# Performance work log

Measured on AMD Instinct MI355X. Metric: run time of the kernel, lower is better.

The kernel has to match this reference:

```python
import jax, jax.numpy as jnp
import numpy as np

N_NODES = 50000
N_EDGES = 800000  # includes N_NODES self-loops so every node has in-degree >= 1
D_IN = 64
D_OUT = 64


def setup_inputs() -> dict:
    key = jax.random.key(0)
    k_feat, k_src, k_dst, k_wt, k_wp = jax.random.split(key, 5)
    feat = jax.random.normal(k_feat, (N_NODES, D_IN), dtype=jnp.float32)
    n_rand = N_EDGES - N_NODES
    loops = jnp.arange(N_NODES, dtype=jnp.int64)
    src = jnp.concatenate([loops, jax.random.randint(k_src, (n_rand,), 0, N_NODES, dtype=jnp.int64)])
    dst = jnp.concatenate([loops, jax.random.randint(k_dst, (n_rand,), 0, N_NODES, dtype=jnp.int64)])
    scale = 1.0 / np.sqrt(D_IN)
    W_theta = jax.random.normal(k_wt, (D_IN, D_OUT), dtype=jnp.float32) * scale
    b_theta = jnp.zeros((D_OUT,), dtype=jnp.float32)
    W_phi = jax.random.normal(k_wp, (D_IN, D_OUT), dtype=jnp.float32) * scale
    b_phi = jnp.zeros((D_OUT,), dtype=jnp.float32)
    return {"feat": feat, "src": src, "dst": dst,
            "W_theta": W_theta, "b_theta": b_theta,
            "W_phi": W_phi, "b_phi": b_phi}


def reference(feat, src, dst, W_theta, b_theta, W_phi, b_phi):
    # Per-edge message: theta(x_dst - x_src)  [fn.v_sub_u then Dense theta]
    diff = feat[dst] - feat[src]                       # [E, D_in]
    theta_e = diff @ W_theta + b_theta                 # [E, D_out]
    # Per-destination-node term: phi(x_dst)  [Dense phi]
    phi = feat @ W_phi + b_phi                         # [N, D_out]
    e = theta_e + phi[dst]                             # [E, D_out]  (fn.e_add_v)
    # Scatter-max aggregation by destination node (fn.max)
    out = jax.ops.segment_max(e, dst, num_segments=feat.shape[0])  # [N, D_out]
    return out
```

## Files before the change

kernel.cpp:

```cpp
#include <hip/hip_runtime.h>
#include <hip/hip_bf16.h>

#define N_NODES 50000
#define N_EDGES 800000
#define D 64
#define NB 1563
#define BCAP 1024
#define CHUNK_E 4096
#define NSC 196
#define NSTRIP 3125
#define GEMM_BLKS 196
#define NWAVES 784
#define SPW 4
#define MSTR 65
#define WLSTR 72
#define NRES 7

typedef __attribute__((ext_vector_type(8))) short short8v;
typedef __attribute__((ext_vector_type(4))) float float4v;

__device__ __forceinline__ float b2f(unsigned short h) {
    return __uint_as_float(((unsigned)h) << 16);
}
__device__ __forceinline__ unsigned short f2b(float f) {
    __hip_bfloat16 t = __float2bfloat16(f);
    return *reinterpret_cast<unsigned short*>(&t);
}
__device__ __forceinline__ unsigned f2ord(float f) {
    unsigned u = __float_as_uint(f);
    return (u & 0x80000000u) ? ~u : (u | 0x80000000u);
}
__device__ __forceinline__ float ord2f(unsigned o) {
    return __uint_as_float((o & 0x80000000u) ? (o ^ 0x80000000u) : ~o);
}

__global__ __launch_bounds__(256)
void gemm_scatter(const void* __restrict__ featv,
                  const void* __restrict__ srcv, const void* __restrict__ dstv,
                  const void* __restrict__ Wtv, const void* __restrict__ btv,
                  const void* __restrict__ Wpv, const void* __restrict__ bpv,
                  unsigned* __restrict__ c_cur, unsigned* __restrict__ packed,
                  unsigned short* __restrict__ T16, void* __restrict__ outv) {
    __shared__ __align__(16) unsigned short wt_l[64 * WLSTR];
    __shared__ __align__(16) unsigned short wp_l[64 * WLSTR];
    __shared__ __align__(16) float bias_l[64];
    __shared__ unsigned h[NB];
    __shared__ unsigned sf[2];
    const int t = threadIdx.x;

    if (t < 64) {
        const unsigned short* p = (const unsigned short*)featv;
        float x = b2f(p[2 * t]);
        float a = fabsf(x);
        bool insane = !(a <= 64.f) || (x != 0.f && a < 9.3132e-10f);
        unsigned long long mm = __ballot(insane);
        if (t == 0) sf[0] = (__popcll(mm) >= 8) ? 1u : 0u;
    } else if (t < 128) {
        const int* s32 = (const int*)srcv;
        int v = s32[2 * (t - 64) + 1];
        unsigned long long mm = __ballot(v == 0);
        if (t == 64) sf[1] = (__popcll(mm) >= 32) ? 1u : 0u;
    }
    __syncthreads();
    const unsigned fp32mode = sf[0];
    const unsigned idx64 = sf[1];

    if (blockIdx.x < GEMM_BLKS) {
        if (fp32mode) {
#pragma unroll
            for (int i = 0; i < 16; ++i) {
                int e = i * 256 + t;
                int k = e >> 6, n = e & 63;
                wt_l[n * WLSTR + k] = f2b(((const float*)Wtv)[e]);
                wp_l[n * WLSTR + k] = f2b(((const float*)Wpv)[e]);
            }
        } else {
#pragma unroll
            for (int i = 0; i < 16; ++i) {
                int e = i * 256 + t;
                int k = e >> 6, n = e & 63;
                wt_l[n * WLSTR + k] = ((const unsigned short*)Wtv)[e];
                wp_l[n * WLSTR + k] = ((const unsigned short*)Wpv)[e];
            }
        }
        if (t < 64) {
            float bt_, bp_;
            if (fp32mode) {
                bt_ = ((const float*)btv)[t];
                bp_ = ((const float*)bpv)[t];
            } else {
                bt_ = b2f(((const unsigned short*)btv)[t]);
                bp_ = b2f(((const unsigned short*)bpv)[t]);
            }
            bias_l[t] = bt_ + bp_;
        }
        __syncthreads();

        const int lane = t & 63, wid = t >> 6;
        const int wave = blockIdx.x * 4 + wid;
        const int m = lane & 15, q = lane >> 4;
        short8v Wt0[4], Wt1[4], Wp0[4], Wp1[4];
        float4 bs4[4];
#pragma unroll
        for (int c = 0; c < 4; ++c) {
            const int col = 16 * c + m;
            Wt0[c] = *(const short8v*)&wt_l[col * WLSTR + q * 8];
            Wt1[c] = *(const short8v*)&wt_l[col * WLSTR + 32 + q * 8];
            Wp0[c] = *(const short8v*)&wp_l[col * WLSTR + q * 8];
            Wp1[c] = *(const short8v*)&wp_l[col * WLSTR + 32 + q * 8];
            bs4[c] = *(const float4*)&bias_l[16 * c + 4 * q];
        }

        float* Cf  = (float*)outv;
        unsigned short* Ch = (unsigned short*)outv;
        const float* Ff = (const float*)featv;
        const short* Fh = (const short*)featv;

        short8v A0, A1;
        float4 raw[8];
        int w = wave;
        {
            int wc = min(w, NSTRIP - 1);
            const short* fr = Fh + (wc * 16 + m) * D + q * 8;
            const float* frf = Ff + (wc * 16 + m) * D + q * 8;
            if (fp32mode) {
                raw[0] = *(const float4*)(frf);      raw[1] = *(const float4*)(frf + 4);
                raw[2] = *(const float4*)(frf + 32); raw[3] = *(const float4*)(frf + 36);
                A0 = (short8v){(short)f2b(raw[0].x), (short)f2b(raw[0].y), (short)f2b(raw[0].z), (short)f2b(raw[0].w),
                               (short)f2b(raw[1].x), (short)f2b(raw[1].y), (short)f2b(raw[1].z), (short)f2b(raw[1].w)};
                A1 = (short8v){(short)f2b(raw[2].x), (short)f2b(raw[2].y), (short)f2b(raw[2].z), (short)f2b(raw[2].w),
                               (short)f2b(raw[3].x), (short)f2b(raw[3].y), (short)f2b(raw[3].z), (short)f2b(raw[3].w)};
            } else {
                A0 = *(const short8v*)fr;
                A1 = *(const short8v*)(fr + 32);
            }
        }

#pragma unroll
        for (int s = 0; s < SPW; ++s) {
            const int wn = wave + (s + 1) * NWAVES;
            if (s + 1 < SPW) {
                int wc = min(wn, NSTRIP - 1);
                if (fp32mode) {
                    const float* frf = Ff + (wc * 16 + m) * D + q * 8;
                    raw[0] = *(const float4*)(frf);      raw[1] = *(const float4*)(frf + 4);
                    raw[2] = *(const float4*)(frf + 32); raw[3] = *(const float4*)(frf + 36);
                } else {
                    const short* fr = Fh + (wc * 16 + m) * D + q * 8;
                    A0 = *(const short8v*)fr;
                    A1 = *(const short8v*)(fr + 32);
                }
            }
            if (w < NSTRIP) {
                short8v Acur0, Acur1;
                if (s + 1 < SPW && !fp32mode) {
                    const short* fr = Fh + (w * 16 + m) * D + q * 8;
                    Acur0 = *(const short8v*)fr;
                    Acur1 = *(const short8v*)(fr + 32);
                } else {
                    Acur0 = A0; Acur1 = A1;
                }
                const int node = w * 16 + m;
                unsigned short* Trow = T16 + node * D;
#pragma unroll
                for (int c = 0; c < 4; ++c) {
                    float4v accT = (float4v){0.f, 0.f, 0.f, 0.f};
                    float4v accP = (float4v){bs4[c].x, bs4[c].y, bs4[c].z, bs4[c].w};
                    accT = __builtin_amdgcn_mfma_f32_16x16x32_bf16(Wt0[c], Acur0, accT, 0, 0, 0);
                    accT = __builtin_amdgcn_mfma_f32_16x16x32_bf16(Wt1[c], Acur1, accT, 0, 0, 0);
                    accP = __builtin_amdgcn_mfma_f32_16x16x32_bf16(Wp0[c], Acur0, accP, 0, 0, 0);
                    accP = __builtin_amdgcn_mfma_f32_16x16x32_bf16(Wp1[c], Acur1, accP, 0, 0, 0);
                    const int foff = 16 * c + 4 * q;
                    unsigned t0 = (unsigned)f2b(accT[0]) | ((unsigned)f2b(accT[1]) << 16);
                    unsigned t1 = (unsigned)f2b(accT[2]) | ((unsigned)f2b(accT[3]) << 16);
                    *(uint2*)(Trow + foff) = make_uint2(t0, t1);
                    if (fp32mode) {
                        *(float4*)(Cf + node * D + foff) =
                            make_float4(accT[0] + accP[0], accT[1] + accP[1],
                                        accT[2] + accP[2], accT[3] + accP[3]);
                    } else {
                        unsigned c0 = (unsigned)f2b(accT[0] + accP[0])
                                    | ((unsigned)f2b(accT[1] + accP[1]) << 16);
                        unsigned c1 = (unsigned)f2b(accT[2] + accP[2])
                                    | ((unsigned)f2b(accT[3] + accP[3]) << 16);
                        *(uint2*)(Ch + node * D + foff) = make_uint2(c0, c1);
                    }
                }
            }
            w = wn;
            if (fp32mode && s + 1 < SPW) {
                A0 = (short8v){(short)f2b(raw[0].x), (short)f2b(raw[0].y), (short)f2b(raw[0].z), (short)f2b(raw[0].w),
                               (short)f2b(raw[1].x), (short)f2b(raw[1].y), (short)f2b(raw[1].z), (short)f2b(raw[1].w)};
                A1 = (short8v){(short)f2b(raw[2].x), (short)f2b(raw[2].y), (short)f2b(raw[2].z), (short)f2b(raw[2].w),
                               (short)f2b(raw[3].x), (short)f2b(raw[3].y), (short)f2b(raw[3].z), (short)f2b(raw[3].w)};
            }
        }
    } else {
        for (int i = t; i < NB; i += 256) h[i] = 0;
        __syncthreads();
        const int base = (blockIdx.x - GEMM_BLKS) * CHUNK_E;
        unsigned pk[CHUNK_E / 256];
#pragma unroll
        for (int j = 0; j < CHUNK_E / 256; ++j) {
            int e = base + j * 256 + t;
            unsigned p = 0xFFFFFFFFu;
            if (e < N_EDGES) {
                int s, d;
                if (idx64) {
                    s = (int)((const long long*)srcv)[e];
                    d = (int)((const long long*)dstv)[e];
                } else {
                    s = ((const int*)srcv)[e];
                    d = ((const int*)dstv)[e];
                }
                s = min(max(s, 0), N_NODES - 1);
                d = min(max(d, 0), N_NODES - 1);
                if (s != d) {
                    p = ((unsigned)d << 16) | (unsigned)s;
                    atomicAdd(&h[d >> 5], 1u);
                }
            }
            pk[j] = p;
        }
        __syncthreads();
        {
            unsigned cc[NRES], off[NRES];
#pragma unroll
            for (int r = 0; r < NRES; ++r) {
                int i = r * 256 + t;
                cc[r] = (i < NB) ? h[i] : 0u;
            }
#pragma unroll
            for (int r = 0; r < NRES; ++r) {
                int i = r * 256 + t;
                off[r] = (i < NB && cc[r]) ? atomicAdd(&c_cur[i], cc[r]) : 0u;
            }
            __syncthreads();
#pragma unroll
            for (int r = 0; r < NRES; ++r) {
                int i = r * 256 + t;
                if (i < NB) h[i] = off[r];
            }
        }
        __syncthreads();
#pragma unroll
        for (int j = 0; j < CHUNK_E / 256; ++j) {
            unsigned p = pk[j];
            if (p != 0xFFFFFFFFu) {
                unsigned bkt = p >> 21;
                unsigned pos = atomicAdd(&h[bkt], 1u);
                if (pos < BCAP)
                    packed[bkt * BCAP + pos] = p;
            }
        }
    }
}

__global__ __launch_bounds__(256, 8)
void bucket_min(const unsigned* __restrict__ c_cur, const unsigned* __restrict__ packed,
                const unsigned short* __restrict__ T16, const void* __restrict__ featv,
                void* __restrict__ outv) {
    __shared__ unsigned mn[32 * MSTR];
    __shared__ unsigned sf0;
    const int t = threadIdx.x;
    const int b = blockIdx.x;
    const int node0 = b << 5;
    if (t < 64) {
        const unsigned short* p = (const unsigned short*)featv;
        float x = b2f(p[2 * t]);
        float a = fabsf(x);
        bool insane = !(a <= 64.f) || (x != 0.f && a < 9.3132e-10f);
        unsigned long long mm = __ballot(insane);
        if (t == 0) sf0 = (__popcll(mm) >= 8) ? 1u : 0u;
    }
    for (int sl = t; sl < 32 * 16; sl += 256) {
        const int row = sl >> 4;
        const int f4 = (sl & 15) << 2;
        unsigned* mp = &mn[row * MSTR + f4];
        if (node0 + row < N_NODES) {
            uint2 v = *(const uint2*)(T16 + (node0 + row) * D + f4);
            mp[0] = f2ord(b2f((unsigned short)v.x));
            mp[1] = f2ord(b2f((unsigned short)(v.x >> 16)));
            mp[2] = f2ord(b2f((unsigned short)v.y));
            mp[3] = f2ord(b2f((unsigned short)(v.y >> 16)));
        } else {
            mp[0] = mp[1] = mp[2] = mp[3] = 0xFFFFFFFFu;
        }
    }
    __syncthreads();
    const unsigned fp32mode = sf0;
    const int cnt = min((int)c_cur[b], BCAP);
    const unsigned* pb = packed + b * BCAP;
    const int lane = t & 63, wv = t >> 6;
    const int g = lane >> 3;
    const int fh = (lane & 7) << 3;
    int i = wv * 8 + g;
    for (; i + 32 < cnt; i += 64) {
        unsigned p0 = pb[i], p1 = pb[i + 32];
        uint4 v0 = *(const uint4*)(T16 + (int)(p0 & 0xFFFFu) * D + fh);
        uint4 v1 = *(const uint4*)(T16 + (int)(p1 & 0xFFFFu) * D + fh);
        unsigned* m0p = &mn[(int)((p0 >> 16) & 31u) * MSTR + fh];
        unsigned* m1p = &mn[(int)((p1 >> 16) & 31u) * MSTR + fh];
        atomicMin(m0p + 0, f2ord(b2f((unsigned short)v0.x)));
        atomicMin(m0p + 1, f2ord(b2f((unsigned short)(v0.x >> 16))));
        atomicMin(m0p + 2, f2ord(b2f((unsigned short)v0.y)));
        atomicMin(m0p + 3, f2ord(b2f((unsigned short)(v0.y >> 16))));
        atomicMin(m0p + 4, f2ord(b2f((unsigned short)v0.z)));
        atomicMin(m0p + 5, f2ord(b2f((unsigned short)(v0.z >> 16))));
        atomicMin(m0p + 6, f2ord(b2f((unsigned short)v0.w)));
        atomicMin(m0p + 7, f2ord(b2f((unsigned short)(v0.w >> 16))));
        atomicMin(m1p + 0, f2ord(b2f((unsigned short)v1.x)));
        atomicMin(m1p + 1, f2ord(b2f((unsigned short)(v1.x >> 16))));
        atomicMin(m1p + 2, f2ord(b2f((unsigned short)v1.y)));
        atomicMin(m1p + 3, f2ord(b2f((unsigned short)(v1.y >> 16))));
        atomicMin(m1p + 4, f2ord(b2f((unsigned short)v1.z)));
        atomicMin(m1p + 5, f2ord(b2f((unsigned short)(v1.z >> 16))));
        atomicMin(m1p + 6, f2ord(b2f((unsigned short)v1.w)));
        atomicMin(m1p + 7, f2ord(b2f((unsigned short)(v1.w >> 16))));
    }
    for (; i < cnt; i += 32) {
        unsigned p0 = pb[i];
        uint4 v0 = *(const uint4*)(T16 + (int)(p0 & 0xFFFFu) * D + fh);
        unsigned* m0p = &mn[(int)((p0 >> 16) & 31u) * MSTR + fh];
        atomicMin(m0p + 0, f2ord(b2f((unsigned short)v0.x)));
        atomicMin(m0p + 1, f2ord(b2f((unsigned short)(v0.x >> 16))));
        atomicMin(m0p + 2, f2ord(b2f((unsigned short)v0.y)));
        atomicMin(m0p + 3, f2ord(b2f((unsigned short)(v0.y >> 16))));
        atomicMin(m0p + 4, f2ord(b2f((unsigned short)v0.z)));
        atomicMin(m0p + 5, f2ord(b2f((unsigned short)(v0.z >> 16))));
        atomicMin(m0p + 6, f2ord(b2f((unsigned short)v0.w)));
        atomicMin(m0p + 7, f2ord(b2f((unsigned short)(v0.w >> 16))));
    }
    __syncthreads();
    for (int sl = t; sl < 32 * 16; sl += 256) {
        const int row = sl >> 4;
        const int node = node0 + row;
        if (node >= N_NODES) continue;
        const int f4 = (sl & 15) << 2;
        const unsigned* mp = &mn[row * MSTR + f4];
        float m0 = ord2f(mp[0]), m1 = ord2f(mp[1]);
        float m2 = ord2f(mp[2]), m3 = ord2f(mp[3]);
        if (fp32mode) {
            float4* C = (float4*)((float*)outv + node * D + f4);
            float4 c = *C;
            *C = make_float4(c.x - m0, c.y - m1, c.z - m2, c.w - m3);
        } else {
            unsigned short* C = (unsigned short*)outv + node * D + f4;
            uint2 c = *(uint2*)C;
            unsigned lo = (unsigned)f2b(b2f((unsigned short)c.x) - m0)
                        | ((unsigned)f2b(b2f((unsigned short)(c.x >> 16)) - m1) << 16);
            unsigned hi = (unsigned)f2b(b2f((unsigned short)c.y) - m2)
                        | ((unsigned)f2b(b2f((unsigned short)(c.y >> 16)) - m3) << 16);
            *(uint2*)C = make_uint2(lo, hi);
        }
    }
}

__global__ __launch_bounds__(256)
void zero_ccur(unsigned* __restrict__ c_cur) {
    int i = blockIdx.x * 256 + threadIdx.x;
    if (i < NB) c_cur[i] = 0;
}

extern "C" void kernel_launch(void* const* d_in, const int* in_sizes, int n_in,
                              void* d_out, int out_size, void* d_ws, size_t ws_size,
                              hipStream_t stream) {
    char* p = (char*)d_ws;
    unsigned*       c_cur  = (unsigned*)p;
    unsigned*       packed = (unsigned*)(p + 8192);
    unsigned short* T16    = (unsigned short*)(p + 8192 + 6402048);

    hipError_t e = hipMemsetAsync(c_cur, 0, NB * sizeof(unsigned), stream);
    if (e != hipSuccess)
        zero_ccur<<<(NB + 255) / 256, 256, 0, stream>>>(c_cur);

    gemm_scatter<<<GEMM_BLKS + NSC, 256, 0, stream>>>(d_in[0], d_in[1], d_in[2],
                                                      d_in[3], d_in[4], d_in[5], d_in[6],
                                                      c_cur, packed, T16, d_out);
    bucket_min<<<NB, 256, 0, stream>>>(c_cur, packed, T16, d_in[0], d_out);
}
```

Before: 113.4 us.

## Make every block do both GEMM strips and edge bucketing

Before, the fused kernel split its blocks into two kinds: GEMM blocks and edge-scatter blocks. Now every one of 512 blocks loads its slice of edge indices up front, computes up to two 16-node GEMM strips, then does local histogramming and the scatter into packed buckets. The aim is to balance work across all CUs and to hide the index-load latency behind the MFMA work. In exchange every block stages the weights into LDS, and register pressure rises from the held edge indices under launch_bounds(256,2).

```diff
diff --git a/kernel.cpp b/kernel.cpp
--- a/kernel.cpp
+++ b/kernel.cpp
@@ -6,15 +6,14 @@
 #define D 64
 #define NB 1563
 #define BCAP 1024
-#define CHUNK_E 4096
-#define NSC 196
 #define NSTRIP 3125
-#define GEMM_BLKS 196
-#define NWAVES 784
-#define SPW 4
 #define MSTR 65
 #define WLSTR 72
 #define NRES 7
+#define K1_BLKS 512
+#define WAVES_G 2048
+#define EPB1 1568
+#define EJ 7
 
 typedef __attribute__((ext_vector_type(8))) short short8v;
 typedef __attribute__((ext_vector_type(4))) float float4v;
@@ -34,7 +33,7 @@
     return __uint_as_float((o & 0x80000000u) ? (o ^ 0x80000000u) : ~o);
 }
 
-__global__ __launch_bounds__(256)
+__global__ __launch_bounds__(256, 2)
 void gemm_scatter(const void* __restrict__ featv,
                   const void* __restrict__ srcv, const void* __restrict__ dstv,
                   const void* __restrict__ Wtv, const void* __restrict__ btv,
@@ -61,43 +60,58 @@
         unsigned long long mm = __ballot(v == 0);
         if (t == 64) sf[1] = (__popcll(mm) >= 32) ? 1u : 0u;
     }
+    for (int i = t; i < NB; i += 256) h[i] = 0;
     __syncthreads();
     const unsigned fp32mode = sf[0];
     const unsigned idx64 = sf[1];
 
-    if (blockIdx.x < GEMM_BLKS) {
+    if (fp32mode) {
+#pragma unroll
+        for (int i = 0; i < 16; ++i) {
+            int e = i * 256 + t;
+            int k = e >> 6, n = e & 63;
+            wt_l[n * WLSTR + k] = f2b(((const float*)Wtv)[e]);
+            wp_l[n * WLSTR + k] = f2b(((const float*)Wpv)[e]);
+        }
+    } else {
+#pragma unroll
+        for (int i = 0; i < 16; ++i) {
+            int e = i * 256 + t;
+            int k = e >> 6, n = e & 63;
+            wt_l[n * WLSTR + k] = ((const unsigned short*)Wtv)[e];
+            wp_l[n * WLSTR + k] = ((const unsigned short*)Wpv)[e];
+        }
+    }
+    if (t < 64) {
+        float bt_, bp_;
         if (fp32mode) {
-#pragma unroll
-            for (int i = 0; i < 16; ++i) {
-                int e = i * 256 + t;
-                int k = e >> 6, n = e & 63;
-                wt_l[n * WLSTR + k] = f2b(((const float*)Wtv)[e]);
-                wp_l[n * WLSTR + k] = f2b(((const float*)Wpv)[e]);
-            }
+            bt_ = ((const float*)btv)[t];
+            bp_ = ((const float*)bpv)[t];
         } else {
-#pragma unroll
-            for (int i = 0; i < 16; ++i) {
-                int e = i * 256 + t;
-                int k = e >> 6, n = e & 63;
-                wt_l[n * WLSTR + k] = ((const unsigned short*)Wtv)[e];
-                wp_l[n * WLSTR + k] = ((const unsigned short*)Wpv)[e];
-            }
-        }
-        if (t < 64) {
-            float bt_, bp_;
-            if (fp32mode) {
-                bt_ = ((const float*)btv)[t];
-                bp_ = ((const float*)bpv)[t];
-            } else {
-                bt_ = b2f(((const unsigned short*)btv)[t]);
-                bp_ = b2f(((const unsigned short*)bpv)[t]);
-            }
-            bias_l[t] = bt_ + bp_;
-        }
-        __syncthreads();
-
+            bt_ = b2f(((const unsigned short*)btv)[t]);
+            bp_ = b2f(((const unsigned short*)bpv)[t]);
+        }
+        bias_l[t] = bt_ + bp_;
+    }
+
+    const int base = blockIdx.x * EPB1;
+    int es[EJ], ed[EJ];
+#pragma unroll
+    for (int j = 0; j < EJ; ++j) {
+        int el = min(base + j * 256 + t, N_EDGES - 1);
+        if (idx64) {
+            es[j] = (int)((const long long*)srcv)[el];
+            ed[j] = (int)((const long long*)dstv)[el];
+        } else {
+            es[j] = ((const int*)srcv)[el];
+            ed[j] = ((const int*)dstv)[el];
+        }
+    }
+    __syncthreads();
+
+    {
         const int lane = t & 63, wid = t >> 6;
-        const int wave = blockIdx.x * 4 + wid;
+        const int wg = blockIdx.x * 4 + wid;
         const int m = lane & 15, q = lane >> 4;
         short8v Wt0[4], Wt1[4], Wp0[4], Wp1[4];
         float4 bs4[4];
@@ -110,66 +124,47 @@
             Wp1[c] = *(const short8v*)&wp_l[col * WLSTR + 32 + q * 8];
             bs4[c] = *(const float4*)&bias_l[16 * c + 4 * q];
         }
-
         float* Cf  = (float*)outv;
         unsigned short* Ch = (unsigned short*)outv;
         const float* Ff = (const float*)featv;
         const short* Fh = (const short*)featv;
 
-        short8v A0, A1;
-        float4 raw[8];
-        int w = wave;
-        {
-            int wc = min(w, NSTRIP - 1);
-            const short* fr = Fh + (wc * 16 + m) * D + q * 8;
-            const float* frf = Ff + (wc * 16 + m) * D + q * 8;
-            if (fp32mode) {
-                raw[0] = *(const float4*)(frf);      raw[1] = *(const float4*)(frf + 4);
-                raw[2] = *(const float4*)(frf + 32); raw[3] = *(const float4*)(frf + 36);
-                A0 = (short8v){(short)f2b(raw[0].x), (short)f2b(raw[0].y), (short)f2b(raw[0].z), (short)f2b(raw[0].w),
-                               (short)f2b(raw[1].x), (short)f2b(raw[1].y), (short)f2b(raw[1].z), (short)f2b(raw[1].w)};
-                A1 = (short8v){(short)f2b(raw[2].x), (short)f2b(raw[2].y), (short)f2b(raw[2].z), (short)f2b(raw[2].w),
-                               (short)f2b(raw[3].x), (short)f2b(raw[3].y), (short)f2b(raw[3].z), (short)f2b(raw[3].w)};
-            } else {
-                A0 = *(const short8v*)fr;
-                A1 = *(const short8v*)(fr + 32);
-            }
-        }
-
-#pragma unroll
-        for (int s = 0; s < SPW; ++s) {
-            const int wn = wave + (s + 1) * NWAVES;
-            if (s + 1 < SPW) {
-                int wc = min(wn, NSTRIP - 1);
+        short8v A0[2], A1[2];
+#pragma unroll
+        for (int k = 0; k < 2; ++k) {
+            const int s = wg + k * WAVES_G;
+            if (s < NSTRIP) {
                 if (fp32mode) {
-                    const float* frf = Ff + (wc * 16 + m) * D + q * 8;
-                    raw[0] = *(const float4*)(frf);      raw[1] = *(const float4*)(frf + 4);
-                    raw[2] = *(const float4*)(frf + 32); raw[3] = *(const float4*)(frf + 36);
+                    const float* frf = Ff + (s * 16 + m) * D + q * 8;
+                    float4 r0 = *(const float4*)(frf);
+                    float4 r1 = *(const float4*)(frf + 4);
+                    float4 r2 = *(const float4*)(frf + 32);
+                    float4 r3 = *(const float4*)(frf + 36);
+                    A0[k] = (short8v){(short)f2b(r0.x), (short)f2b(r0.y), (short)f2b(r0.z), (short)f2b(r0.w),
+                                      (short)f2b(r1.x), (short)f2b(r1.y), (short)f2b(r1.z), (short)f2b(r1.w)};
+                    A1[k] = (short8v){(short)f2b(r2.x), (short)f2b(r2.y), (short)f2b(r2.z), (short)f2b(r2.w),
+                                      (short)f2b(r3.x), (short)f2b(r3.y), (short)f2b(r3.z), (short)f2b(r3.w)};
                 } else {
-                    const short* fr = Fh + (wc * 16 + m) * D + q * 8;
-                    A0 = *(const short8v*)fr;
-                    A1 = *(const short8v*)(fr + 32);
+                    const short* fr = Fh + (s * 16 + m) * D + q * 8;
+                    A0[k] = *(const short8v*)fr;
+                    A1[k] = *(const short8v*)(fr + 32);
                 }
             }
-            if (w < NSTRIP) {
-                short8v Acur0, Acur1;
-                if (s + 1 < SPW && !fp32mode) {
-                    const short* fr = Fh + (w * 16 + m) * D + q * 8;
-                    Acur0 = *(const short8v*)fr;
-                    Acur1 = *(const short8v*)(fr + 32);
-                } else {
-                    Acur0 = A0; Acur1 = A1;
-                }
-                const int node = w * 16 + m;
+        }
+#pragma unroll
+        for (int k = 0; k < 2; ++k) {
+            const int s = wg + k * WAVES_G;
+            if (s < NSTRIP) {
+                const int node = s * 16 + m;
                 unsigned short* Trow = T16 + node * D;
 #pragma unroll
                 for (int c = 0; c < 4; ++c) {
                     float4v accT = (float4v){0.f, 0.f, 0.f, 0.f};
                     float4v accP = (float4v){bs4[c].x, bs4[c].y, bs4[c].z, bs4[c].w};
-                    accT = __builtin_amdgcn_mfma_f32_16x16x32_bf16(Wt0[c], Acur0, accT, 0, 0, 0);
-                    accT = __builtin_amdgcn_mfma_f32_16x16x32_bf16(Wt1[c], Acur1, accT, 0, 0, 0);
-                    accP = __builtin_amdgcn_mfma_f32_16x16x32_bf16(Wp0[c], Acur0, accP, 0, 0, 0);
-                    accP = __builtin_amdgcn_mfma_f32_16x16x32_bf16(Wp1[c], Acur1, accP, 0, 0, 0);
+                    accT = __builtin_amdgcn_mfma_f32_16x16x32_bf16(Wt0[c], A0[k], accT, 0, 0, 0);
+                    accT = __builtin_amdgcn_mfma_f32_16x16x32_bf16(Wt1[c], A1[k], accT, 0, 0, 0);
+                    accP = __builtin_amdgcn_mfma_f32_16x16x32_bf16(Wp0[c], A0[k], accP, 0, 0, 0);
+                    accP = __builtin_amdgcn_mfma_f32_16x16x32_bf16(Wp1[c], A1[k], accP, 0, 0, 0);
                     const int foff = 16 * c + 4 * q;
                     unsigned t0 = (unsigned)f2b(accT[0]) | ((unsigned)f2b(accT[1]) << 16);
                     unsigned t1 = (unsigned)f2b(accT[2]) | ((unsigned)f2b(accT[3]) << 16);
@@ -187,71 +182,53 @@
                     }
                 }
             }
-            w = wn;
-            if (fp32mode && s + 1 < SPW) {
-                A0 = (short8v){(short)f2b(raw[0].x), (short)f2b(raw[0].y), (short)f2b(raw[0].z), (short)f2b(raw[0].w),
-                               (short)f2b(raw[1].x), (short)f2b(raw[1].y), (short)f2b(raw[1].z), (short)f2b(raw[1].w)};
-                A1 = (short8v){(short)f2b(raw[2].x), (short)f2b(raw[2].y), (short)f2b(raw[2].z), (short)f2b(raw[2].w),
-                               (short)f2b(raw[3].x), (short)f2b(raw[3].y), (short)f2b(raw[3].z), (short)f2b(raw[3].w)};
+        }
+    }
+
+    unsigned pk[EJ];
+#pragma unroll
+    for (int j = 0; j < EJ; ++j) {
+        const int li = j * 256 + t;
+        unsigned p = 0xFFFFFFFFu;
+        if (li < EPB1 && base + li < N_EDGES) {
+            int s = min(max(es[j], 0), N_NODES - 1);
+            int d = min(max(ed[j], 0), N_NODES - 1);
+            if (s != d) {
+                p = ((unsigned)d << 16) | (unsigned)s;
+                atomicAdd(&h[d >> 5], 1u);
             }
         }
-    } else {
-        for (int i = t; i < NB; i += 256) h[i] = 0;
+        pk[j] = p;
+    }
+    __syncthreads();
+    {
+        unsigned cc[NRES], off[NRES];
+#pragma unroll
+        for (int r = 0; r < NRES; ++r) {
+            int i = r * 256 + t;
+            cc[r] = (i < NB) ? h[i] : 0u;
+        }
+#pragma unroll
+        for (int r = 0; r < NRES; ++r) {
+            int i = r * 256 + t;
+            off[r] = (i < NB && cc[r]) ? atomicAdd(&c_cur[i], cc[r]) : 0u;
+        }
         __syncthreads();
-        const int base = (blockIdx.x - GEMM_BLKS) * CHUNK_E;
-        unsigned pk[CHUNK_E / 256];
-#pragma unroll
-        for (int j = 0; j < CHUNK_E / 256; ++j) {
-            int e = base + j * 256 + t;
-            unsigned p = 0xFFFFFFFFu;
-            if (e < N_EDGES) {
-                int s, d;
-                if (idx64) {
-                    s = (int)((const long long*)srcv)[e];
-                    d = (int)((const long long*)dstv)[e];
-                } else {
-                    s = ((const int*)srcv)[e];
-                    d = ((const int*)dstv)[e];
-                }
-                s = min(max(s, 0), N_NODES - 1);
-                d = min(max(d, 0), N_NODES - 1);
-                if (s != d) {
-                    p = ((unsigned)d << 16) | (unsigned)s;
-                    atomicAdd(&h[d >> 5], 1u);
-                }
-            }
-            pk[j] = p;
-        }
-        __syncthreads();
-        {
-            unsigned cc[NRES], off[NRES];
-#pragma unroll
-            for (int r = 0; r < NRES; ++r) {
-                int i = r * 256 + t;
-                cc[r] = (i < NB) ? h[i] : 0u;
-            }
-#pragma unroll
-            for (int r = 0; r < NRES; ++r) {
-                int i = r * 256 + t;
-                off[r] = (i < NB && cc[r]) ? atomicAdd(&c_cur[i], cc[r]) : 0u;
-            }
-            __syncthreads();
-#pragma unroll
-            for (int r = 0; r < NRES; ++r) {
-                int i = r * 256 + t;
-                if (i < NB) h[i] = off[r];
-            }
-        }
-        __syncthreads();
-#pragma unroll
-        for (int j = 0; j < CHUNK_E / 256; ++j) {
-            unsigned p = pk[j];
-            if (p != 0xFFFFFFFFu) {
-                unsigned bkt = p >> 21;
-                unsigned pos = atomicAdd(&h[bkt], 1u);
-                if (pos < BCAP)
-                    packed[bkt * BCAP + pos] = p;
-            }
+#pragma unroll
+        for (int r = 0; r < NRES; ++r) {
+            int i = r * 256 + t;
+            if (i < NB) h[i] = off[r];
+        }
+    }
+    __syncthreads();
+#pragma unroll
+    for (int j = 0; j < EJ; ++j) {
+        unsigned p = pk[j];
+        if (p != 0xFFFFFFFFu) {
+            unsigned bkt = p >> 21;
+            unsigned pos = atomicAdd(&h[bkt], 1u);
+            if (pos < BCAP)
+                packed[bkt * BCAP + pos] = p;
         }
     }
 }
@@ -374,8 +351,8 @@
     if (e != hipSuccess)
         zero_ccur<<<(NB + 255) / 256, 256, 0, stream>>>(c_cur);
 
-    gemm_scatter<<<GEMM_BLKS + NSC, 256, 0, stream>>>(d_in[0], d_in[1], d_in[2],
-                                                      d_in[3], d_in[4], d_in[5], d_in[6],
-                                                      c_cur, packed, T16, d_out);
+    gemm_scatter<<<K1_BLKS, 256, 0, stream>>>(d_in[0], d_in[1], d_in[2],
+                                              d_in[3], d_in[4], d_in[5], d_in[6],
+                                              c_cur, packed, T16, d_out);
     bucket_min<<<NB, 256, 0, stream>>>(c_cur, packed, T16, d_in[0], d_out);
 }
```

New measurement: 118.8 us. 4.8% more time.

## Store order-preserving bf16 keys in T16 and skip redundant LDS atomics

Applied to the files above, without the earlier changes.

The GEMM stage now writes the theta values as order-preserving 16-bit keys. The bucket_min kernel can then build its 32-bit min keys with a shift or mask, with no float decode and re-encode per element. Before each shared-memory atomicMin, it reads the current minimum with vectorized LDS loads and issues the atomic only when the new key is smaller. The row stride changes from 65 to 66 so those uint2 reads stay aligned. This cuts ALU work and atomic traffic in the edge loop, at the cost of extra LDS reads, and the skip check may race with other lanes, which is harmless for a min.

```diff
diff --git a/kernel.cpp b/kernel.cpp
--- a/kernel.cpp
+++ b/kernel.cpp
@@ -12,7 +12,7 @@
 #define GEMM_BLKS 196
 #define NWAVES 784
 #define SPW 4
-#define MSTR 65
+#define MSTR 66
 #define WLSTR 72
 #define NRES 7
 
@@ -26,12 +26,14 @@
     __hip_bfloat16 t = __float2bfloat16(f);
     return *reinterpret_cast<unsigned short*>(&t);
 }
-__device__ __forceinline__ unsigned f2ord(float f) {
-    unsigned u = __float_as_uint(f);
-    return (u & 0x80000000u) ? ~u : (u | 0x80000000u);
-}
-__device__ __forceinline__ float ord2f(unsigned o) {
-    return __uint_as_float((o & 0x80000000u) ? (o ^ 0x80000000u) : ~o);
+__device__ __forceinline__ unsigned short ord16(unsigned short b) {
+    return (b & 0x8000u) ? (unsigned short)~b : (unsigned short)(b | 0x8000u);
+}
+__device__ __forceinline__ float ord16_dec(unsigned o32) {
+    unsigned short o = (unsigned short)(o32 >> 16);
+    unsigned short b = (o & 0x8000u) ? (unsigned short)(o ^ 0x8000u)
+                                     : (unsigned short)~o;
+    return b2f(b);
 }
 
 __global__ __launch_bounds__(256)
@@ -171,8 +173,10 @@
                     accP = __builtin_amdgcn_mfma_f32_16x16x32_bf16(Wp0[c], Acur0, accP, 0, 0, 0);
                     accP = __builtin_amdgcn_mfma_f32_16x16x32_bf16(Wp1[c], Acur1, accP, 0, 0, 0);
                     const int foff = 16 * c + 4 * q;
-                    unsigned t0 = (unsigned)f2b(accT[0]) | ((unsigned)f2b(accT[1]) << 16);
-                    unsigned t1 = (unsigned)f2b(accT[2]) | ((unsigned)f2b(accT[3]) << 16);
+                    unsigned t0 = (unsigned)ord16(f2b(accT[0]))
+                                | ((unsigned)ord16(f2b(accT[1])) << 16);
+                    unsigned t1 = (unsigned)ord16(f2b(accT[2]))
+                                | ((unsigned)ord16(f2b(accT[3])) << 16);
                     *(uint2*)(Trow + foff) = make_uint2(t0, t1);
                     if (fp32mode) {
                         *(float4*)(Cf + node * D + foff) =
@@ -255,6 +259,21 @@
         }
     }
 }
+
+#define EDGE_MIN(vv, mp)                                                    \
+    do {                                                                    \
+        uint2 ca = *(const uint2*)((mp) + 0), cb = *(const uint2*)((mp) + 2); \
+        uint2 cc_ = *(const uint2*)((mp) + 4), cd = *(const uint2*)((mp) + 6); \
+        unsigned o;                                                         \
+        o = (vv).x << 16;          if (o < ca.x) atomicMin((mp) + 0, o);    \
+        o = (vv).x & 0xFFFF0000u;  if (o < ca.y) atomicMin((mp) + 1, o);    \
+        o = (vv).y << 16;          if (o < cb.x) atomicMin((mp) + 2, o);    \
+        o = (vv).y & 0xFFFF0000u;  if (o < cb.y) atomicMin((mp) + 3, o);    \
+        o = (vv).z << 16;          if (o < cc_.x) atomicMin((mp) + 4, o);   \
+        o = (vv).z & 0xFFFF0000u;  if (o < cc_.y) atomicMin((mp) + 5, o);   \
+        o = (vv).w << 16;          if (o < cd.x) atomicMin((mp) + 6, o);    \
+        o = (vv).w & 0xFFFF0000u;  if (o < cd.y) atomicMin((mp) + 7, o);    \
+    } while (0)
 
 __global__ __launch_bounds__(256, 8)
 void bucket_min(const unsigned* __restrict__ c_cur, const unsigned* __restrict__ packed,
@@ -279,10 +298,10 @@
         unsigned* mp = &mn[row * MSTR + f4];
         if (node0 + row < N_NODES) {
             uint2 v = *(const uint2*)(T16 + (node0 + row) * D + f4);
-            mp[0] = f2ord(b2f((unsigned short)v.x));
-            mp[1] = f2ord(b2f((unsigned short)(v.x >> 16)));
-            mp[2] = f2ord(b2f((unsigned short)v.y));
-            mp[3] = f2ord(b2f((unsigned short)(v.y >> 16)));
+            mp[0] = v.x << 16;
+            mp[1] = v.x & 0xFFFF0000u;
+            mp[2] = v.y << 16;
+            mp[3] = v.y & 0xFFFF0000u;
         } else {
             mp[0] = mp[1] = mp[2] = mp[3] = 0xFFFFFFFFu;
         }
@@ -301,35 +320,14 @@
         uint4 v1 = *(const uint4*)(T16 + (int)(p1 & 0xFFFFu) * D + fh);
         unsigned* m0p = &mn[(int)((p0 >> 16) & 31u) * MSTR + fh];
         unsigned* m1p = &mn[(int)((p1 >> 16) & 31u) * MSTR + fh];
-        atomicMin(m0p + 0, f2ord(b2f((unsigned short)v0.x)));
-        atomicMin(m0p + 1, f2ord(b2f((unsigned short)(v0.x >> 16))));
-        atomicMin(m0p + 2, f2ord(b2f((unsigned short)v0.y)));
-        atomicMin(m0p + 3, f2ord(b2f((unsigned short)(v0.y >> 16))));
-        atomicMin(m0p + 4, f2ord(b2f((unsigned short)v0.z)));
-        atomicMin(m0p + 5, f2ord(b2f((unsigned short)(v0.z >> 16))));
-        atomicMin(m0p + 6, f2ord(b2f((unsigned short)v0.w)));
-        atomicMin(m0p + 7, f2ord(b2f((unsigned short)(v0.w >> 16))));
-        atomicMin(m1p + 0, f2ord(b2f((unsigned short)v1.x)));
-        atomicMin(m1p + 1, f2ord(b2f((unsigned short)(v1.x >> 16))));
-        atomicMin(m1p + 2, f2ord(b2f((unsigned short)v1.y)));
-        atomicMin(m1p + 3, f2ord(b2f((unsigned short)(v1.y >> 16))));
-        atomicMin(m1p + 4, f2ord(b2f((unsigned short)v1.z)));
-        atomicMin(m1p + 5, f2ord(b2f((unsigned short)(v1.z >> 16))));
-        atomicMin(m1p + 6, f2ord(b2f((unsigned short)v1.w)));
-        atomicMin(m1p + 7, f2ord(b2f((unsigned short)(v1.w >> 16))));
+        EDGE_MIN(v0, m0p);
+        EDGE_MIN(v1, m1p);
     }
     for (; i < cnt; i += 32) {
         unsigned p0 = pb[i];
         uint4 v0 = *(const uint4*)(T16 + (int)(p0 & 0xFFFFu) * D + fh);
         unsigned* m0p = &mn[(int)((p0 >> 16) & 31u) * MSTR + fh];
-        atomicMin(m0p + 0, f2ord(b2f((unsigned short)v0.x)));
-        atomicMin(m0p + 1, f2ord(b2f((unsigned short)(v0.x >> 16))));
-        atomicMin(m0p + 2, f2ord(b2f((unsigned short)v0.y)));
-        atomicMin(m0p + 3, f2ord(b2f((unsigned short)(v0.y >> 16))));
-        atomicMin(m0p + 4, f2ord(b2f((unsigned short)v0.z)));
-        atomicMin(m0p + 5, f2ord(b2f((unsigned short)(v0.z >> 16))));
-        atomicMin(m0p + 6, f2ord(b2f((unsigned short)v0.w)));
-        atomicMin(m0p + 7, f2ord(b2f((unsigned short)(v0.w >> 16))));
+        EDGE_MIN(v0, m0p);
     }
     __syncthreads();
     for (int sl = t; sl < 32 * 16; sl += 256) {
@@ -338,8 +336,8 @@
         if (node >= N_NODES) continue;
         const int f4 = (sl & 15) << 2;
         const unsigned* mp = &mn[row * MSTR + f4];
-        float m0 = ord2f(mp[0]), m1 = ord2f(mp[1]);
-        float m2 = ord2f(mp[2]), m3 = ord2f(mp[3]);
+        float m0 = ord16_dec(mp[0]), m1 = ord16_dec(mp[1]);
+        float m2 = ord16_dec(mp[2]), m3 = ord16_dec(mp[3]);
         if (fp32mode) {
             float4* C = (float4*)((float*)outv + node * D + f4);
             float4 c = *C;
```

Result: slower. 116.3 us (+2.6%).
